# Optimization experiments

Hardware: AMD Instinct MI355X
Metric: run time of the kernel (lower is better)

## Reference

```python
import jax, jax.numpy as jnp
import numpy as np

DIM = 64
N_EMBED = 1024
POS_DIM = 16
POS_EMBED = 128


def _build_mask(dim, n_embed, pos_dim, pos_embed):
    # mask[dim-pos_dim:, :n_embed-pos_embed] = 0 ; mask[:dim-pos_dim, n_embed-pos_embed:] = 0
    m = np.ones((dim, n_embed), dtype=np.float32)
    m[dim - pos_dim:, : n_embed - pos_embed] = 0.0
    m[: dim - pos_dim, n_embed - pos_embed:] = 0.0
    return jnp.asarray(m)


def setup_inputs() -> dict:
    key = jax.random.key(0)
    k1, k2 = jax.random.split(key)
    inp = jax.random.normal(k1, (64, 32, 32, DIM), dtype=jnp.float32)  # [B,H,W,dim]
    embed = jax.random.normal(k2, (DIM, N_EMBED), dtype=jnp.float32)   # codebook buffer
    return {"input": inp, "embed": embed, "bi": 1}


def reference(input, embed, bi):
    dim, n_embed = embed.shape
    mask = _build_mask(dim, n_embed, POS_DIM, POS_EMBED)
    embed_m = embed * mask  # self.embed = embed * mask

    # select codebook columns depending on branch
    if bi == 1:
        cols = embed_m                              # [dim, n_embed]
    else:
        cols = embed_m[:, : n_embed - POS_EMBED]    # [dim, n_embed - pos_embed]

    flatten = input.reshape(-1, dim)  # [N, dim]
    # squared euclidean distance: ||f||^2 - 2 f.e + ||e||^2
    dist = (
        jnp.sum(flatten * flatten, axis=1, keepdims=True)
        - 2.0 * flatten @ cols
        + jnp.sum(cols * cols, axis=0, keepdims=True)
    )  # [N, K]
    embed_ind = jnp.argmin(dist, axis=1)                 # argmax of -dist
    embed_ind = embed_ind.reshape(input.shape[:-1])      # [B,H,W]

    # embedding lookup: F.embedding(ind, cols.T)
    quantize = jnp.take(cols.T, embed_ind, axis=0)       # [B,H,W,dim]

    diff = jnp.mean(
        (jax.lax.stop_gradient(quantize) - input) ** 2, axis=(1, 2, 3)
    )  # [B]
    quantize_st = input + jax.lax.stop_gradient(quantize - input)  # straight-through
    return (quantize_st, diff, embed_ind, embed_m)
```

## Files before the change

### kernel.cpp

```cpp
#include <hip/hip_runtime.h>

#define N_ROWS 65536
#define DIM    64
#define NE     1024
#define NPOS   128
#define KSPLIT 48

#define OFF_DIFF  (N_ROWS * DIM)
#define OFF_IND   (OFF_DIFF + 64)
#define OFF_EMBM  (OFF_IND + N_ROWS)


__global__ __launch_bounds__(64) void k_prep(const float* __restrict__ embed,
                                             float* __restrict__ out,
                                             float* __restrict__ colsT,
                                             float* __restrict__ cnh) {
    int c = blockIdx.x * 64 + threadIdx.x;
    bool clow = c < (NE - NPOS);
    float s = 0.f;
#pragma unroll
    for (int j = 0; j < DIM / 4; ++j) {
        float v0 = embed[(4 * j + 0) * NE + c];
        float v1 = embed[(4 * j + 1) * NE + c];
        float v2 = embed[(4 * j + 2) * NE + c];
        float v3 = embed[(4 * j + 3) * NE + c];
        v0 = (((4 * j + 0) < KSPLIT) == clow) ? v0 : 0.f;
        v1 = (((4 * j + 1) < KSPLIT) == clow) ? v1 : 0.f;
        v2 = (((4 * j + 2) < KSPLIT) == clow) ? v2 : 0.f;
        v3 = (((4 * j + 3) < KSPLIT) == clow) ? v3 : 0.f;
        out[OFF_EMBM + (4 * j + 0) * NE + c] = v0;
        out[OFF_EMBM + (4 * j + 1) * NE + c] = v1;
        out[OFF_EMBM + (4 * j + 2) * NE + c] = v2;
        out[OFF_EMBM + (4 * j + 3) * NE + c] = v3;
        colsT[c * DIM + 4 * j + 0] = v0;
        colsT[c * DIM + 4 * j + 1] = v1;
        colsT[c * DIM + 4 * j + 2] = v2;
        colsT[c * DIM + 4 * j + 3] = v3;
        s += v0 * v0 + v1 * v1 + v2 * v2 + v3 * v3;
    }
    cnh[c] = 0.5f * s;
    if (c < 64) out[OFF_DIFF + c] = 0.f;
}

#define FMA4(XJ, V) { a0 += XJ.x * V.x; a1 += XJ.y * V.y; a2 += XJ.z * V.z; a3 += XJ.w * V.w; }

#define DOT_A_LDS(CP, OUT) { \
    float a0 = 0.f, a1 = 0.f, a2 = 0.f, a3 = 0.f; float4 v; \
    v = CP[0];  FMA4(x0,  v); \
    v = CP[1];  FMA4(x1,  v); \
    v = CP[2];  FMA4(x2,  v); \
    v = CP[3];  FMA4(x3,  v); \
    v = CP[4];  FMA4(x4,  v); \
    v = CP[5];  FMA4(x5,  v); \
    v = CP[6];  FMA4(x6,  v); \
    v = CP[7];  FMA4(x7,  v); \
    v = CP[8];  FMA4(x8,  v); \
    v = CP[9];  FMA4(x9,  v); \
    v = CP[10]; FMA4(x10, v); \
    v = CP[11]; FMA4(x11, v); \
    OUT = (a0 + a1) + (a2 + a3); }

#define DOT_B_LDS(CP, OUT) { \
    float a0 = 0.f, a1 = 0.f, a2 = 0.f, a3 = 0.f; float4 v; \
    v = CP[12]; FMA4(x12, v); \
    v = CP[13]; FMA4(x13, v); \
    v = CP[14]; FMA4(x14, v); \
    v = CP[15]; FMA4(x15, v); \
    OUT = (a0 + a1) + (a2 + a3); }

#define TAKE(SC, C) { float a_ = (SC) - cnh[(C)]; bool g_ = a_ > best; \
    best = g_ ? a_ : best; bidx = g_ ? (C) : bidx; }

__global__ __launch_bounds__(256, 4) void k_main(const float* __restrict__ input,
                                                 const float* __restrict__ colsT,
                                                 const float* __restrict__ cnh,
                                                 float* __restrict__ out) {
    const int wave = __builtin_amdgcn_readfirstlane(threadIdx.x >> 6);
    const int lane = threadIdx.x & 63;
    const int row  = blockIdx.x * 64 + lane;

    __shared__ float4 lds4[4 * 32 * 16];
    __shared__ float  sbest[4][64];
    __shared__ int    sidx[4][64];

    const float4* __restrict__ xp = (const float4*)(input + (size_t)row * DIM);
    float4 x0  = xp[0],  x1  = xp[1],  x2  = xp[2],  x3  = xp[3];
    float4 x4  = xp[4],  x5  = xp[5],  x6  = xp[6],  x7  = xp[7];
    float4 x8  = xp[8],  x9  = xp[9],  x10 = xp[10], x11 = xp[11];
    float4 x12 = xp[12], x13 = xp[13], x14 = xp[14], x15 = xp[15];

    float best = -3.0e38f;
    int   bidx = 0;

    const float4* __restrict__ colsT4 = (const float4*)colsT;
    float4* __restrict__ ldst = lds4 + wave * 512;

    for (int i = 0; i < 7; ++i) {
        const int cb = 224 * wave + 32 * i;
#pragma unroll
        for (int t = 0; t < 8; ++t)
            ldst[t * 64 + lane] = colsT4[(size_t)cb * 16 + t * 64 + lane];
#pragma unroll 2
        for (int j = 0; j < 32; j += 4) {
            const float4* __restrict__ cp0 = ldst + (j + 0) * 16;
            const float4* __restrict__ cp1 = ldst + (j + 1) * 16;
            const float4* __restrict__ cp2 = ldst + (j + 2) * 16;
            const float4* __restrict__ cp3 = ldst + (j + 3) * 16;
            float s0, s1, s2, s3;
            DOT_A_LDS(cp0, s0);
            DOT_A_LDS(cp1, s1);
            DOT_A_LDS(cp2, s2);
            DOT_A_LDS(cp3, s3);
            TAKE(s0, cb + j + 0);
            TAKE(s1, cb + j + 1);
            TAKE(s2, cb + j + 2);
            TAKE(s3, cb + j + 3);
        }
    }

    {
        const int cb = (NE - NPOS) + 32 * wave;
#pragma unroll
        for (int t = 0; t < 8; ++t)
            ldst[t * 64 + lane] = colsT4[(size_t)cb * 16 + t * 64 + lane];
#pragma unroll 2
        for (int j = 0; j < 32; j += 4) {
            const float4* __restrict__ cp0 = ldst + (j + 0) * 16;
            const float4* __restrict__ cp1 = ldst + (j + 1) * 16;
            const float4* __restrict__ cp2 = ldst + (j + 2) * 16;
            const float4* __restrict__ cp3 = ldst + (j + 3) * 16;
            float s0, s1, s2, s3;
            DOT_B_LDS(cp0, s0);
            DOT_B_LDS(cp1, s1);
            DOT_B_LDS(cp2, s2);
            DOT_B_LDS(cp3, s3);
            TAKE(s0, cb + j + 0);
            TAKE(s1, cb + j + 1);
            TAKE(s2, cb + j + 2);
            TAKE(s3, cb + j + 3);
        }
    }

    sbest[wave][lane] = best;
    sidx[wave][lane]  = bidx;
    __syncthreads();

    if (wave == 0) {
        float b  = sbest[0][lane];
        int   bi = sidx[0][lane];
#pragma unroll
        for (int w = 1; w < 4; ++w) {
            float bw = sbest[w][lane];
            int   iw = sidx[w][lane];
            bool g = (bw > b) || (bw == b && iw < bi);
            b  = g ? bw : b;
            bi = g ? iw : bi;
        }

        const float4* __restrict__ qp = (const float4*)(colsT + bi * DIM);
        float4* __restrict__ oq = (float4*)(out + (size_t)row * DIM);
        float s = 0.f;
#define EPI(J, XJ) { float4 q = qp[J]; \
        float d0 = q.x - XJ.x, d1 = q.y - XJ.y, d2 = q.z - XJ.z, d3 = q.w - XJ.w; \
        float4 r; r.x = XJ.x + d0; r.y = XJ.y + d1; r.z = XJ.z + d2; r.w = XJ.w + d3; \
        oq[J] = r; s += d0 * d0 + d1 * d1 + d2 * d2 + d3 * d3; }
        EPI(0,  x0);  EPI(1,  x1);  EPI(2,  x2);  EPI(3,  x3);
        EPI(4,  x4);  EPI(5,  x5);  EPI(6,  x6);  EPI(7,  x7);
        EPI(8,  x8);  EPI(9,  x9);  EPI(10, x10); EPI(11, x11);
        EPI(12, x12); EPI(13, x13); EPI(14, x14); EPI(15, x15);
#undef EPI

        out[OFF_IND + row] = (float)bi;

#pragma unroll
        for (int off = 32; off > 0; off >>= 1)
            s += __shfl_down(s, off, 64);
        if (lane == 0)
            atomicAdd(out + OFF_DIFF + (blockIdx.x >> 4),
                      s * (1.0f / (32.0f * 32.0f * 64.0f)));
    }
}

extern "C" void kernel_launch(void* const* d_in, const int* in_sizes, int n_in,
                              void* d_out, int out_size, void* d_ws, size_t ws_size,
                              hipStream_t stream) {
    const float* input = (const float*)d_in[0];
    const float* embed = (const float*)d_in[1];

    float* out   = (float*)d_out;
    float* colsT = (float*)d_ws;
    float* cnh   = colsT + NE * DIM;

    k_prep<<<16, 64, 0, stream>>>(embed, out, colsT, cnh);
    k_main<<<1024, 256, 0, stream>>>(input, colsT, cnh, out);
}
```

Before: 215.9 us.

## Split each row's dot products across two lanes with shuffle reduction

Each input row is handled by a pair of lanes, each holding half of the 64-dimensional vector, and the partial dot products are summed with a cross-lane shuffle. Blocks cover 32 rows instead of 64, the grid doubles, and the codebook LDS tiles shrink to 16 codes. The aim is to cut per-thread registers and raise parallelism and occupancy. The cost is extra shuffle and duplicated argmin work per code, plus more codebook traffic per row.

```diff
diff --git a/kernel.cpp b/kernel.cpp
--- a/kernel.cpp
+++ b/kernel.cpp
@@ -42,75 +42,67 @@
     if (c < 64) out[OFF_DIFF + c] = 0.f;
 }
 
-#define FMA4(XJ, V) { a0 += XJ.x * V.x; a1 += XJ.y * V.y; a2 += XJ.z * V.z; a3 += XJ.w * V.w; }
+#define DOTPA(CP, OUT) { float a0 = 0.f, a1 = 0.f; float4 v; \
+    v = CP[0];  a0 += xa0.x * v.x; a1 += xa0.y * v.y; a0 += xa0.z * v.z; a1 += xa0.w * v.w; \
+    v = CP[2];  a0 += xa1.x * v.x; a1 += xa1.y * v.y; a0 += xa1.z * v.z; a1 += xa1.w * v.w; \
+    v = CP[4];  a0 += xa2.x * v.x; a1 += xa2.y * v.y; a0 += xa2.z * v.z; a1 += xa2.w * v.w; \
+    v = CP[6];  a0 += xa3.x * v.x; a1 += xa3.y * v.y; a0 += xa3.z * v.z; a1 += xa3.w * v.w; \
+    v = CP[8];  a0 += xa4.x * v.x; a1 += xa4.y * v.y; a0 += xa4.z * v.z; a1 += xa4.w * v.w; \
+    v = CP[10]; a0 += xa5.x * v.x; a1 += xa5.y * v.y; a0 += xa5.z * v.z; a1 += xa5.w * v.w; \
+    OUT = a0 + a1; }
 
-#define DOT_A_LDS(CP, OUT) { \
-    float a0 = 0.f, a1 = 0.f, a2 = 0.f, a3 = 0.f; float4 v; \
-    v = CP[0];  FMA4(x0,  v); \
-    v = CP[1];  FMA4(x1,  v); \
-    v = CP[2];  FMA4(x2,  v); \
-    v = CP[3];  FMA4(x3,  v); \
-    v = CP[4];  FMA4(x4,  v); \
-    v = CP[5];  FMA4(x5,  v); \
-    v = CP[6];  FMA4(x6,  v); \
-    v = CP[7];  FMA4(x7,  v); \
-    v = CP[8];  FMA4(x8,  v); \
-    v = CP[9];  FMA4(x9,  v); \
-    v = CP[10]; FMA4(x10, v); \
-    v = CP[11]; FMA4(x11, v); \
-    OUT = (a0 + a1) + (a2 + a3); }
-
-#define DOT_B_LDS(CP, OUT) { \
-    float a0 = 0.f, a1 = 0.f, a2 = 0.f, a3 = 0.f; float4 v; \
-    v = CP[12]; FMA4(x12, v); \
-    v = CP[13]; FMA4(x13, v); \
-    v = CP[14]; FMA4(x14, v); \
-    v = CP[15]; FMA4(x15, v); \
-    OUT = (a0 + a1) + (a2 + a3); }
+#define DOTPB(CP, OUT) { float a0 = 0.f, a1 = 0.f; float4 v; \
+    v = CP[12]; a0 += xb0.x * v.x; a1 += xb0.y * v.y; a0 += xb0.z * v.z; a1 += xb0.w * v.w; \
+    v = CP[14]; a0 += xb1.x * v.x; a1 += xb1.y * v.y; a0 += xb1.z * v.z; a1 += xb1.w * v.w; \
+    OUT = a0 + a1; }
 
 #define TAKE(SC, C) { float a_ = (SC) - cnh[(C)]; bool g_ = a_ > best; \
     best = g_ ? a_ : best; bidx = g_ ? (C) : bidx; }
 
-__global__ __launch_bounds__(256, 4) void k_main(const float* __restrict__ input,
-                                                 const float* __restrict__ colsT,
-                                                 const float* __restrict__ cnh,
-                                                 float* __restrict__ out) {
+__global__ __launch_bounds__(256) void k_main(const float* __restrict__ input,
+                                              const float* __restrict__ colsT,
+                                              const float* __restrict__ cnh,
+                                              float* __restrict__ out) {
     const int wave = __builtin_amdgcn_readfirstlane(threadIdx.x >> 6);
     const int lane = threadIdx.x & 63;
-    const int row  = blockIdx.x * 64 + lane;
+    const int half = lane & 1;
+    const int row  = blockIdx.x * 32 + (lane >> 1);
 
-    __shared__ float4 lds4[4 * 32 * 16];
+    __shared__ float4 lds4[4 * 256];
     __shared__ float  sbest[4][64];
     __shared__ int    sidx[4][64];
 
-    const float4* __restrict__ xp = (const float4*)(input + (size_t)row * DIM);
-    float4 x0  = xp[0],  x1  = xp[1],  x2  = xp[2],  x3  = xp[3];
-    float4 x4  = xp[4],  x5  = xp[5],  x6  = xp[6],  x7  = xp[7];
-    float4 x8  = xp[8],  x9  = xp[9],  x10 = xp[10], x11 = xp[11];
-    float4 x12 = xp[12], x13 = xp[13], x14 = xp[14], x15 = xp[15];
+    const float4* __restrict__ xq = (const float4*)(input + (size_t)row * DIM);
+    float4 xa0 = xq[0  + half], xa1 = xq[2  + half], xa2 = xq[4  + half];
+    float4 xa3 = xq[6  + half], xa4 = xq[8  + half], xa5 = xq[10 + half];
+    float4 xb0 = xq[12 + half], xb1 = xq[14 + half];
 
     float best = -3.0e38f;
     int   bidx = 0;
 
     const float4* __restrict__ colsT4 = (const float4*)colsT;
-    float4* __restrict__ ldst = lds4 + wave * 512;
+    float4* __restrict__ ldst = lds4 + wave * 256;
 
-    for (int i = 0; i < 7; ++i) {
-        const int cb = 224 * wave + 32 * i;
+    for (int i = 0; i < 14; ++i) {
+        const int cb = 224 * wave + 16 * i;
 #pragma unroll
-        for (int t = 0; t < 8; ++t)
+        for (int t = 0; t < 4; ++t)
             ldst[t * 64 + lane] = colsT4[(size_t)cb * 16 + t * 64 + lane];
 #pragma unroll 2
-        for (int j = 0; j < 32; j += 4) {
-            const float4* __restrict__ cp0 = ldst + (j + 0) * 16;
-            const float4* __restrict__ cp1 = ldst + (j + 1) * 16;
-            const float4* __restrict__ cp2 = ldst + (j + 2) * 16;
-            const float4* __restrict__ cp3 = ldst + (j + 3) * 16;
-            float s0, s1, s2, s3;
-            DOT_A_LDS(cp0, s0);
-            DOT_A_LDS(cp1, s1);
-            DOT_A_LDS(cp2, s2);
-            DOT_A_LDS(cp3, s3);
+        for (int j = 0; j < 16; j += 4) {
+            const float4* __restrict__ cp0 = ldst + (j + 0) * 16 + half;
+            const float4* __restrict__ cp1 = ldst + (j + 1) * 16 + half;
+            const float4* __restrict__ cp2 = ldst + (j + 2) * 16 + half;
+            const float4* __restrict__ cp3 = ldst + (j + 3) * 16 + half;
+            float p0, p1, p2, p3;
+            DOTPA(cp0, p0);
+            DOTPA(cp1, p1);
+            DOTPA(cp2, p2);
+            DOTPA(cp3, p3);
+            float s0 = p0 + __shfl_xor(p0, 1, 64);
+            float s1 = p1 + __shfl_xor(p1, 1, 64);
+            float s2 = p2 + __shfl_xor(p2, 1, 64);
+            float s3 = p3 + __shfl_xor(p3, 1, 64);
             TAKE(s0, cb + j + 0);
             TAKE(s1, cb + j + 1);
             TAKE(s2, cb + j + 2);
@@ -118,22 +110,26 @@
         }
     }
 
-    {
-        const int cb = (NE - NPOS) + 32 * wave;
+    for (int i = 0; i < 2; ++i) {
+        const int cb = (NE - NPOS) + 32 * wave + 16 * i;
 #pragma unroll
-        for (int t = 0; t < 8; ++t)
+        for (int t = 0; t < 4; ++t)
             ldst[t * 64 + lane] = colsT4[(size_t)cb * 16 + t * 64 + lane];
 #pragma unroll 2
-        for (int j = 0; j < 32; j += 4) {
-            const float4* __restrict__ cp0 = ldst + (j + 0) * 16;
-            const float4* __restrict__ cp1 = ldst + (j + 1) * 16;
-            const float4* __restrict__ cp2 = ldst + (j + 2) * 16;
-            const float4* __restrict__ cp3 = ldst + (j + 3) * 16;
-            float s0, s1, s2, s3;
-            DOT_B_LDS(cp0, s0);
-            DOT_B_LDS(cp1, s1);
-            DOT_B_LDS(cp2, s2);
-            DOT_B_LDS(cp3, s3);
+        for (int j = 0; j < 16; j += 4) {
+            const float4* __restrict__ cp0 = ldst + (j + 0) * 16 + half;
+            const float4* __restrict__ cp1 = ldst + (j + 1) * 16 + half;
+            const float4* __restrict__ cp2 = ldst + (j + 2) * 16 + half;
+            const float4* __restrict__ cp3 = ldst + (j + 3) * 16 + half;
+            float p0, p1, p2, p3;
+            DOTPB(cp0, p0);
+            DOTPB(cp1, p1);
+            DOTPB(cp2, p2);
+            DOTPB(cp3, p3);
+            float s0 = p0 + __shfl_xor(p0, 1, 64);
+            float s1 = p1 + __shfl_xor(p1, 1, 64);
+            float s2 = p2 + __shfl_xor(p2, 1, 64);
+            float s3 = p3 + __shfl_xor(p3, 1, 64);
             TAKE(s0, cb + j + 0);
             TAKE(s1, cb + j + 1);
             TAKE(s2, cb + j + 2);
@@ -157,26 +153,25 @@
             bi = g ? iw : bi;
         }
 
-        const float4* __restrict__ qp = (const float4*)(colsT + bi * DIM);
+        const float4* __restrict__ qp = colsT4 + (size_t)bi * 16;
         float4* __restrict__ oq = (float4*)(out + (size_t)row * DIM);
         float s = 0.f;
-#define EPI(J, XJ) { float4 q = qp[J]; \
+#define EPI(CH, XJ) { float4 q = qp[CH]; \
         float d0 = q.x - XJ.x, d1 = q.y - XJ.y, d2 = q.z - XJ.z, d3 = q.w - XJ.w; \
         float4 r; r.x = XJ.x + d0; r.y = XJ.y + d1; r.z = XJ.z + d2; r.w = XJ.w + d3; \
-        oq[J] = r; s += d0 * d0 + d1 * d1 + d2 * d2 + d3 * d3; }
-        EPI(0,  x0);  EPI(1,  x1);  EPI(2,  x2);  EPI(3,  x3);
-        EPI(4,  x4);  EPI(5,  x5);  EPI(6,  x6);  EPI(7,  x7);
-        EPI(8,  x8);  EPI(9,  x9);  EPI(10, x10); EPI(11, x11);
-        EPI(12, x12); EPI(13, x13); EPI(14, x14); EPI(15, x15);
+        oq[CH] = r; s += d0 * d0 + d1 * d1 + d2 * d2 + d3 * d3; }
+        EPI(0  + half, xa0); EPI(2  + half, xa1); EPI(4  + half, xa2);
+        EPI(6  + half, xa3); EPI(8  + half, xa4); EPI(10 + half, xa5);
+        EPI(12 + half, xb0); EPI(14 + half, xb1);
 #undef EPI
 
-        out[OFF_IND + row] = (float)bi;
+        if (half == 0) out[OFF_IND + row] = (float)bi;
 
 #pragma unroll
         for (int off = 32; off > 0; off >>= 1)
             s += __shfl_down(s, off, 64);
         if (lane == 0)
-            atomicAdd(out + OFF_DIFF + (blockIdx.x >> 4),
+            atomicAdd(out + OFF_DIFF + (blockIdx.x >> 5),
                       s * (1.0f / (32.0f * 32.0f * 64.0f)));
     }
 }
@@ -192,5 +187,5 @@
     float* cnh   = colsT + NE * DIM;
 
     k_prep<<<16, 64, 0, stream>>>(embed, out, colsT, cnh);
-    k_main<<<1024, 256, 0, stream>>>(input, colsT, cnh, out);
+    k_main<<<2048, 256, 0, stream>>>(input, colsT, cnh, out);
 }
```

Result: faster. 208.2 us (-3.5%).
